# Performance work log

Measured on AMD Instinct MI355X. Metric: run time of the kernel, lower is better.

## Reference

```python
import jax, jax.numpy as jnp
import numpy as np

B, S, H, NH = 8, 1024, 1024, 16
D = H // NH          # attention_hidden_size = 64
V = S                # v_size must equal seq_len (mask broadcast)


def setup_inputs() -> dict:
    key = jax.random.key(0)
    ks = jax.random.split(key, 9)
    s = 0.02
    return {
        "q": jax.random.normal(ks[0], (B, S, H), jnp.float32),
        "k": jax.random.normal(ks[1], (B, S, H), jnp.float32),
        "v": jax.random.normal(ks[2], (B, S, H), jnp.float32),
        # per-head Q/K projections, stacked over heads: (NH, H, D)
        "Wq": jax.random.normal(ks[3], (NH, H, D), jnp.float32) * s,
        "bq": jax.random.normal(ks[4], (NH, D), jnp.float32) * s,
        "Wk": jax.random.normal(ks[5], (NH, H, D), jnp.float32) * s,
        "bk": jax.random.normal(ks[6], (NH, D), jnp.float32) * s,
        # shared V projection hidden -> v_size
        "Wv": jax.random.normal(ks[7], (H, V), jnp.float32) * s,
        "bv": jax.random.normal(ks[8], (V,), jnp.float32) * s,
    }


def reference(q, k, v, Wq, bq, Wk, bk, Wv, bv):
    d = Wq.shape[-1]
    scale = d ** (-0.5)
    # per-head projections, heads vectorized into leading axis n
    qh = jnp.einsum('bsh,nhd->nbsd', q, Wq) + bq[:, None, None, :]
    kh = jnp.einsum('bth,nhd->nbtd', k, Wk) + bk[:, None, None, :]
    vv = jnp.einsum('bth,hv->btv', v, Wv) + bv          # shared V: (B,S,V)
    seq = q.shape[1]
    mask = jnp.triu(jnp.full((seq, seq), -jnp.inf, dtype=q.dtype), 1)
    scores = jnp.einsum('nbsd,nbtd->nbst', qh, kh) * scale + mask
    p = jax.nn.softmax(scores, axis=-1)                  # (NH,B,S,S)
    # matmul against shared V then mean over heads (== stack + mean)
    out = jnp.einsum('nbst,btv->nbsv', p, vv).mean(axis=0)
    return out
```

## Files before the change

kernel.cpp:

```cpp
#include <hip/hip_runtime.h>


#define NHEAD 16
#define BATCH 8
#define SEQ   1024
#define HID   1024
#define DHEAD 64

typedef _Float16 f16;
typedef _Float16 f16x4 __attribute__((ext_vector_type(4)));
typedef _Float16 f16x8 __attribute__((ext_vector_type(8)));
typedef float    f32x4 __attribute__((ext_vector_type(4)));

__device__ __forceinline__ f32x4 mfma16(f16x8 a, f16x8 b, f32x4 c) {
  return __builtin_amdgcn_mfma_f32_16x16x32_f16(a, b, c, 0, 0, 0);
}

__device__ __forceinline__ void gload16(const f16* g, f16* l) {
  __builtin_amdgcn_global_load_lds(
      (const __attribute__((address_space(1))) void*)g,
      (__attribute__((address_space(3))) void*)l, 16, 0, 0);
}

__device__ __forceinline__ void stage_swz(const f16* __restrict__ g, int ldg,
                                          f16* lds, int nch, int tid,
                                          int step = 256) {
  for (int idx = tid; idx < nch; idx += step) {
    int row = idx >> 3, c16 = idx & 7;
    int sc = c16 ^ (row & 7);
    gload16(g + (size_t)row * ldg + sc * 8, lds + (size_t)(idx & ~63) * 8);
  }
}

__device__ __forceinline__ f16x8 lds_frag(const f16* lds, int row, int c16) {
  int sc = c16 ^ (row & 7);
  return *(const f16x8*)&lds[row * 64 + sc * 8];
}


__global__ __launch_bounds__(256) void conv3(
    const float* __restrict__ q, const float* __restrict__ k,
    const float* __restrict__ v, f16* __restrict__ dq, f16* __restrict__ dk,
    f16* __restrict__ dv) {
  const float* src = blockIdx.z == 0 ? q : blockIdx.z == 1 ? k : v;
  f16* dst = blockIdx.z == 0 ? dq : blockIdx.z == 1 ? dk : dv;
  int i = (blockIdx.x * 256 + threadIdx.x) * 4;
  float4 f = *(const float4*)(src + i);
  f16x4 o = { (f16)f.x, (f16)f.y, (f16)f.z, (f16)f.w };
  *(f16x4*)(dst + i) = o;
}

__global__ __launch_bounds__(256) void tconv2(
    const float* __restrict__ s0, const float* __restrict__ s1,
    f16* __restrict__ d0, f16* __restrict__ d1, int R, int C, int half) {
  int z = blockIdx.z;
  const float* src; f16* dst;
  if (z < half) { src = s0 + (size_t)z * R * C; dst = d0 + (size_t)z * R * C; }
  else { src = s1 + (size_t)(z - half) * R * C; dst = d1 + (size_t)(z - half) * R * C; }
  const int c0 = blockIdx.x * 64, r0 = blockIdx.y * 64;
  __shared__ f16 t[64][72];
  const int tid = threadIdx.x;
#pragma unroll
  for (int i = 0; i < 4; i++) {
    int chunk = tid + i * 256;
    int row = chunk >> 4, c4 = chunk & 15;
    float4 f = *(const float4*)&src[(size_t)(r0 + row) * C + c0 + c4 * 4];
    f16x4 h = { (f16)f.x, (f16)f.y, (f16)f.z, (f16)f.w };
    *(f16x4*)&t[row][c4 * 4] = h;
  }
  __syncthreads();
  const int cc = tid >> 2, q = tid & 3;
  f16 tmp[16];
#pragma unroll
  for (int j = 0; j < 16; j++) tmp[j] = t[q * 16 + j][cc];
  *(f16x8*)&dst[(size_t)(c0 + cc) * R + r0 + q * 16] = *(f16x8*)&tmp[0];
  *(f16x8*)&dst[(size_t)(c0 + cc) * R + r0 + q * 16 + 8] = *(f16x8*)&tmp[8];
}


__device__ __forceinline__ void gemm_core(
    const f16* __restrict__ A, const f16* __restrict__ Bt, int K, int Kend,
    int row0, int col0, f16* la, f16* lb, int tid, f32x4 (&acc)[4][4]) {
  const int lane = tid & 63;
  const int wr = (tid >> 6) >> 1, wc = (tid >> 6) & 1;
  for (int k0 = 0; k0 < Kend; k0 += 64) {
    __syncthreads();
    stage_swz(A + (size_t)row0 * K + k0, K, la, 1024, tid);
    stage_swz(Bt + (size_t)col0 * K + k0, K, lb, 1024, tid);
    __syncthreads();
#pragma unroll
    for (int ks = 0; ks < 2; ks++) {
      f16x8 af[4], bfr[4];
#pragma unroll
      for (int mi = 0; mi < 4; mi++)
        af[mi] = lds_frag(la, wr * 64 + mi * 16 + (lane & 15), ks * 4 + (lane >> 4));
#pragma unroll
      for (int ni = 0; ni < 4; ni++)
        bfr[ni] = lds_frag(lb, wc * 64 + ni * 16 + (lane & 15), ks * 4 + (lane >> 4));
#pragma unroll
      for (int mi = 0; mi < 4; mi++)
#pragma unroll
        for (int ni = 0; ni < 4; ni++)
          acc[mi][ni] = mfma16(af[mi], bfr[ni], acc[mi][ni]);
    }
  }
}


__global__ __launch_bounds__(256) void proj_gemm(
    const f16* __restrict__ A0, const f16* __restrict__ A1,
    const f16* __restrict__ Bt0, const f16* __restrict__ Bt1,
    const float* __restrict__ bias0, const float* __restrict__ bias1,
    f16* __restrict__ C0, f16* __restrict__ C1) {
  const int which = blockIdx.z;
  const f16* A = which ? A1 : A0;
  const f16* Bt = which ? Bt1 : Bt0;
  const float* bias = which ? bias1 : bias0;
  f16* C = which ? C1 : C0;
  __shared__ alignas(16) f16 la[128 * 64];
  __shared__ alignas(16) f16 lb[128 * 64];
  const int tid = threadIdx.x, lane = tid & 63;
  const int wr = (tid >> 6) >> 1, wc = (tid >> 6) & 1;
  const int row0 = blockIdx.x * 128, col0 = blockIdx.y * 128;
  f32x4 acc[4][4];
#pragma unroll
  for (int i = 0; i < 4; i++)
#pragma unroll
    for (int j = 0; j < 4; j++) acc[i][j] = (f32x4){0.f, 0.f, 0.f, 0.f};
  gemm_core(A, Bt, HID, HID, row0, col0, la, lb, tid, acc);
#pragma unroll
  for (int mi = 0; mi < 4; mi++)
#pragma unroll
    for (int ni = 0; ni < 4; ni++)
#pragma unroll
      for (int r = 0; r < 4; r++) {
        int m = row0 + wr * 64 + mi * 16 + ((lane >> 4) << 2) + r;
        int j = col0 + wc * 64 + ni * 16 + (lane & 15);
        float val = acc[mi][ni][r] + bias[j];
        int bb = m >> 10, s = m & 1023, hn = j >> 6, d = j & 63;
        C[(((size_t)hn * BATCH + bb) * SEQ + s) * DHEAD + d] = (f16)val;
      }
}


__global__ __launch_bounds__(256) void vv_gemm(
    const f16* __restrict__ A, const f16* __restrict__ Bt,
    const float* __restrict__ bias, f16* __restrict__ C) {
  __shared__ alignas(16) f16 la[128 * 64];
  __shared__ alignas(16) f16 lb[128 * 64];
  const int tid = threadIdx.x, lane = tid & 63;
  const int wr = (tid >> 6) >> 1, wc = (tid >> 6) & 1;
  const int row0 = blockIdx.x * 128, col0 = blockIdx.y * 128;
  f32x4 acc[4][4];
#pragma unroll
  for (int i = 0; i < 4; i++)
#pragma unroll
    for (int j = 0; j < 4; j++) acc[i][j] = (f32x4){0.f, 0.f, 0.f, 0.f};
  gemm_core(A, Bt, HID, HID, row0, col0, la, lb, tid, acc);
#pragma unroll
  for (int mi = 0; mi < 4; mi++)
#pragma unroll
    for (int ni = 0; ni < 4; ni++)
#pragma unroll
      for (int r = 0; r < 4; r++) {
        int m = row0 + wr * 64 + mi * 16 + ((lane >> 4) << 2) + r;
        int j = col0 + wc * 64 + ni * 16 + (lane & 15);
        float val = acc[mi][ni][r] + bias[m];
        int bb = j >> 10, t = j & 1023;
        C[((size_t)bb * SEQ + m) * SEQ + t] = (f16)val;
      }
}


__global__ __launch_bounds__(256) void attn_stats(
    const f16* __restrict__ QH, const f16* __restrict__ KH,
    float* __restrict__ madj_ws) {
  const int flat = blockIdx.x;
  const int sb = 15 - (flat >> 7);
  const int nb = flat & 127;
  const int n = nb >> 3, b = nb & 7;
  const int s0 = sb * 64;
  const f16* qh = QH + ((size_t)n * BATCH + b) * SEQ * DHEAD;
  const f16* kh = KH + ((size_t)n * BATCH + b) * SEQ * DHEAD;

  const int tid = threadIdx.x, lane = tid & 63, wave = tid >> 6;
  const int lr = lane & 15;
  const int qg = lane >> 4;
  const int ch = qg << 3;

  f16x8 aq[4][2];
#pragma unroll
  for (int fi = 0; fi < 4; fi++) {
    const f16* qp = qh + (size_t)(s0 + fi * 16 + lr) * 64 + ch;
    aq[fi][0] = *(const f16x8*)qp;
    aq[fi][1] = *(const f16x8*)(qp + 32);
  }

  const float sl2e = 0.125f * 1.44269504088896f;
  float l_p[16];
#pragma unroll
  for (int i = 0; i < 16; i++) l_p[i] = 0.f;

  const int nt = (sb + 1) * 4;
  const int dstart = sb * 4;
  const int njw = (nt - wave + 3) >> 2;
  const f16* kp = kh + (size_t)lr * 64 + ch;

  f16x8 kA0, kA1, kB0, kB1;

#define LDK(jj, X0, X1) { const f16* p_ = kp + (size_t)(jj) * 1024; \
    X0 = *(const f16x8*)p_; X1 = *(const f16x8*)(p_ + 32); }

#define COMP(jj, X0, X1) { \
    f32x4 c_[4]; \
    _Pragma("unroll") for (int fi = 0; fi < 4; fi++) { \
      f32x4 cc = (f32x4){0.f, 0.f, 0.f, 0.f}; \
      cc = mfma16(aq[fi][0], X0, cc); cc = mfma16(aq[fi][1], X1, cc); \
      c_[fi] = cc; } \
    if ((jj) < dstart) { \
      _Pragma("unroll") for (int fi = 0; fi < 4; fi++) \
        _Pragma("unroll") for (int r = 0; r < 4; r++) \
          l_p[fi * 4 + r] += exp2f(c_[fi][r] * sl2e); \
    } else { \
      int tg_ = (jj) * 16 + lr; \
      _Pragma("unroll") for (int fi = 0; fi < 4; fi++) \
        _Pragma("unroll") for (int r = 0; r < 4; r++) { \
          int sg_ = s0 + fi * 16 + qg * 4 + r; \
          l_p[fi * 4 + r] += (tg_ <= sg_) ? exp2f(c_[fi][r] * sl2e) : 0.f; } } }

  LDK(wave, kA0, kA1);
  int idx = 0;
  for (; idx + 2 <= njw; idx += 2) {
    LDK(wave + (idx + 1) * 4, kB0, kB1);
    COMP(wave + idx * 4, kA0, kA1);
    if (idx + 2 < njw) LDK(wave + (idx + 2) * 4, kA0, kA1);
    COMP(wave + (idx + 1) * 4, kB0, kB1);
  }
  if (idx < njw) COMP(wave + idx * 4, kA0, kA1);
#undef LDK
#undef COMP

  __shared__ float lds_l[4][64];
#pragma unroll
  for (int i = 0; i < 16; i++) {
    float l = l_p[i];
    l += __shfl_xor(l, 1); l += __shfl_xor(l, 2);
    l += __shfl_xor(l, 4); l += __shfl_xor(l, 8);
    if (lr == 0) lds_l[wave][(i >> 2) * 16 + qg * 4 + (i & 3)] = l;
  }
  __syncthreads();
  if (tid < 64) {
    float l = lds_l[0][tid] + lds_l[1][tid] + lds_l[2][tid] + lds_l[3][tid];
    madj_ws[((size_t)n * BATCH + b) * SEQ + s0 + tid] = -__log2f(l) - 4.0f;
  }
}


__global__ __launch_bounds__(512, 4) void pbar_gemm(
    const f16* __restrict__ QH, const f16* __restrict__ KH,
    const float* __restrict__ madj_ws, f16* __restrict__ pp) {
  const int flat = blockIdx.x;
  const int wg = (flat & 7) * 72 + (flat >> 3);
  const int y = wg / 36;
  int rb = 0, cb = 0;
  {
    int t = wg % 36;
#pragma unroll
    for (int r = 0; r < 8; ++r) {
      if (t <= r) { rb = r; cb = t; break; }
      t -= r + 1;
    }
  }
  const int r0 = rb * 128, c0 = cb * 128;
  const int b = y >> 1, g = y & 1;
  const int n0 = g * 8;
  const bool diag = (rb == cb);

  __shared__ alignas(16) f16 la[2][128 * 64];
  __shared__ alignas(16) f16 lb[2][128 * 64];

  const int tid = threadIdx.x, lane = tid & 63;
  const int wave = tid >> 6;
  const int wr = wave >> 2, wc = wave & 3;
  const int lr = lane & 15, qg = lane >> 4;
  const float sl2e = 0.125f * 1.44269504088896f;
  const size_t HS = (size_t)BATCH * SEQ * DHEAD;
  const f16* qbase = QH + ((size_t)n0 * BATCH + b) * SEQ * DHEAD + (size_t)r0 * 64;
  const f16* kbase = KH + ((size_t)n0 * BATCH + b) * SEQ * DHEAD + (size_t)c0 * 64;
  const float* mbase = madj_ws + ((size_t)n0 * BATCH + b) * SEQ + r0 +
                       wr * 64 + qg * 4;

  f32x4 pacc[4][2];
#pragma unroll
  for (int i = 0; i < 4; i++)
#pragma unroll
    for (int j = 0; j < 2; j++) pacc[i][j] = (f32x4){0.f, 0.f, 0.f, 0.f};

  stage_swz(qbase, 64, la[0], 1024, tid, 512);
  stage_swz(kbase, 64, lb[0], 1024, tid, 512);
  __syncthreads();

  for (int h = 0; h < 8; ++h) {
    const int cur = h & 1;
    if (h + 1 < 8) {
      stage_swz(qbase + (size_t)(h + 1) * HS, 64, la[cur ^ 1], 1024, tid, 512);
      stage_swz(kbase + (size_t)(h + 1) * HS, 64, lb[cur ^ 1], 1024, tid, 512);
    }
    const float* mb = mbase + (size_t)h * BATCH * SEQ;
    float4 m4[4];
#pragma unroll
    for (int mi = 0; mi < 4; mi++) m4[mi] = *(const float4*)(mb + mi * 16);

    f32x4 acc[4][2];
#pragma unroll
    for (int i = 0; i < 4; i++)
#pragma unroll
      for (int j = 0; j < 2; j++) acc[i][j] = (f32x4){0.f, 0.f, 0.f, 0.f};

#pragma unroll
    for (int ks = 0; ks < 2; ks++) {
      f16x8 af[4], bfr[2];
#pragma unroll
      for (int mi = 0; mi < 4; mi++)
        af[mi] = lds_frag(la[cur], wr * 64 + mi * 16 + lr, ks * 4 + qg);
#pragma unroll
      for (int ni = 0; ni < 2; ni++)
        bfr[ni] = lds_frag(lb[cur], wc * 32 + ni * 16 + lr, ks * 4 + qg);
#pragma unroll
      for (int mi = 0; mi < 4; mi++)
#pragma unroll
        for (int ni = 0; ni < 2; ni++)
          acc[mi][ni] = mfma16(af[mi], bfr[ni], acc[mi][ni]);
    }

#pragma unroll
    for (int mi = 0; mi < 4; mi++) {
      float ma[4] = {m4[mi].x, m4[mi].y, m4[mi].z, m4[mi].w};
#pragma unroll
      for (int ni = 0; ni < 2; ni++) {
        int tg = c0 + wc * 32 + ni * 16 + lr;
#pragma unroll
        for (int r = 0; r < 4; r++) {
          float p = exp2f(fmaf(acc[mi][ni][r], sl2e, ma[r]));
          if (diag) {
            int sg = r0 + wr * 64 + mi * 16 + qg * 4 + r;
            p = (tg <= sg) ? p : 0.f;
          }
          pacc[mi][ni][r] += p;
        }
      }
    }
    __syncthreads();
  }

  f16* out = pp + ((size_t)g * BATCH + b) * SEQ * SEQ;
#pragma unroll
  for (int mi = 0; mi < 4; mi++)
#pragma unroll
    for (int ni = 0; ni < 2; ni++)
#pragma unroll
      for (int r = 0; r < 4; r++) {
        int m = r0 + wr * 64 + mi * 16 + qg * 4 + r;
        int j = c0 + wc * 32 + ni * 16 + lr;
        out[(size_t)m * SEQ + j] = (f16)pacc[mi][ni][r];
      }
}


__global__ __launch_bounds__(256) void pv_gemm(
    const f16* __restrict__ pp, const f16* __restrict__ vvT,
    float* __restrict__ out) {
  const int b = blockIdx.z;
  const size_t GS = (size_t)BATCH * SEQ * SEQ;
  const f16* A0 = pp + (size_t)b * SEQ * SEQ;
  const f16* A1 = pp + GS + (size_t)b * SEQ * SEQ;
  const f16* Bt = vvT + (size_t)b * SEQ * SEQ;
  __shared__ alignas(16) f16 la0[128 * 64];
  __shared__ alignas(16) f16 la1[128 * 64];
  __shared__ alignas(16) f16 lb[128 * 64];
  const int tid = threadIdx.x, lane = tid & 63;
  const int wr = (tid >> 6) >> 1, wc = (tid >> 6) & 1;
  const int row0 = blockIdx.x * 128, col0 = blockIdx.y * 128;
  const int Kend = (row0 + 128 < SEQ) ? row0 + 128 : SEQ;

  f32x4 acc[4][4];
#pragma unroll
  for (int i = 0; i < 4; i++)
#pragma unroll
    for (int j = 0; j < 4; j++) acc[i][j] = (f32x4){0.f, 0.f, 0.f, 0.f};

  for (int k0 = 0; k0 < Kend; k0 += 64) {
    __syncthreads();
    stage_swz(A0 + (size_t)row0 * SEQ + k0, SEQ, la0, 1024, tid);
    stage_swz(A1 + (size_t)row0 * SEQ + k0, SEQ, la1, 1024, tid);
    stage_swz(Bt + (size_t)col0 * SEQ + k0, SEQ, lb, 1024, tid);
    __syncthreads();
#pragma unroll
    for (int ks = 0; ks < 2; ks++) {
      f16x8 a0[4], a1[4], bfr[4];
#pragma unroll
      for (int mi = 0; mi < 4; mi++) {
        a0[mi] = lds_frag(la0, wr * 64 + mi * 16 + (lane & 15), ks * 4 + (lane >> 4));
        a1[mi] = lds_frag(la1, wr * 64 + mi * 16 + (lane & 15), ks * 4 + (lane >> 4));
      }
#pragma unroll
      for (int ni = 0; ni < 4; ni++)
        bfr[ni] = lds_frag(lb, wc * 64 + ni * 16 + (lane & 15), ks * 4 + (lane >> 4));
#pragma unroll
      for (int mi = 0; mi < 4; mi++)
#pragma unroll
        for (int ni = 0; ni < 4; ni++) {
          acc[mi][ni] = mfma16(a0[mi], bfr[ni], acc[mi][ni]);
          acc[mi][ni] = mfma16(a1[mi], bfr[ni], acc[mi][ni]);
        }
    }
  }

#pragma unroll
  for (int mi = 0; mi < 4; mi++)
#pragma unroll
    for (int ni = 0; ni < 4; ni++)
#pragma unroll
      for (int r = 0; r < 4; r++) {
        int m = row0 + wr * 64 + mi * 16 + ((lane >> 4) << 2) + r;
        int j = col0 + wc * 64 + ni * 16 + (lane & 15);
        out[(size_t)b * SEQ * SEQ + (size_t)m * SEQ + j] = acc[mi][ni][r];
      }
}


extern "C" void kernel_launch(void* const* d_in, const int* in_sizes, int n_in,
                              void* d_out, int out_size, void* d_ws, size_t ws_size,
                              hipStream_t stream) {
  (void)in_sizes; (void)n_in; (void)out_size; (void)ws_size;
  const float* q  = (const float*)d_in[0];
  const float* k  = (const float*)d_in[1];
  const float* v  = (const float*)d_in[2];
  const float* Wq = (const float*)d_in[3];
  const float* bq = (const float*)d_in[4];
  const float* Wk = (const float*)d_in[5];
  const float* bk = (const float*)d_in[6];
  const float* Wv = (const float*)d_in[7];
  const float* bv = (const float*)d_in[8];
  float* out = (float*)d_out;

  const size_t EL  = (size_t)BATCH * SEQ * HID;
  const size_t WEL = (size_t)NHEAD * HID * DHEAD;

  char* ws = (char*)d_ws;
  f16* qbf = (f16*)ws;  ws += EL * 2;
  f16* kbf = (f16*)ws;  ws += EL * 2;
  f16* vbf = (f16*)ws;  ws += EL * 2;
  f16* WqT = (f16*)ws;  ws += WEL * 2;
  f16* WkT = (f16*)ws;  ws += WEL * 2;
  f16* WvT = (f16*)ws;  ws += WEL * 2;
  f16* QHb = (f16*)ws;  ws += EL * 2;
  f16* KHb = (f16*)ws;  ws += EL * 2;
  f16* vvT = (f16*)ws;  ws += EL * 2;
  float* madj_ws = (float*)ws; ws += (size_t)NHEAD * BATCH * SEQ * 4;
  f16* pp = qbf;

  conv3<<<dim3(8192, 1, 3), 256, 0, stream>>>(q, k, v, qbf, kbf, vbf);
  tconv2<<<dim3(1, 16, 32), 256, 0, stream>>>(Wq, Wk, WqT, WkT, 1024, 64, 16);
  tconv2<<<dim3(16, 16, 1), 256, 0, stream>>>(Wv, Wv, WvT, WvT, 1024, 1024, 1);

  proj_gemm<<<dim3(64, 8, 2), 256, 0, stream>>>(qbf, kbf, WqT, WkT, bq, bk,
                                                QHb, KHb);
  vv_gemm<<<dim3(8, 64, 1), 256, 0, stream>>>(WvT, vbf, bv, vvT);

  attn_stats<<<dim3(2048, 1, 1), 256, 0, stream>>>(QHb, KHb, madj_ws);
  pbar_gemm<<<dim3(576, 1, 1), 512, 0, stream>>>(QHb, KHb, madj_ws, pp);
  pv_gemm<<<dim3(8, 8, 8), 256, 0, stream>>>(pp, vvT, out);
}
```

Measured before the change: 225.8 us.

## Double-buffer LDS and use 8 waves in projection GEMMs

The projection and V GEMMs now use two LDS buffers so the next K-slice loads while MFMAs run on the current one, removing one barrier per step. Blocks grow to 512 threads with each wave owning a 64x32 sub-tile. This aims to hide global-load latency and raise occupancy, at the cost of doubled LDS per block (64KB) and fewer accumulators per wave.

```diff
diff --git a/kernel.cpp b/kernel.cpp
--- a/kernel.cpp
+++ b/kernel.cpp
@@ -78,36 +78,47 @@
 }
 
 
-__device__ __forceinline__ void gemm_core(
+__device__ __forceinline__ void gemm_core512(
     const f16* __restrict__ A, const f16* __restrict__ Bt, int K, int Kend,
-    int row0, int col0, f16* la, f16* lb, int tid, f32x4 (&acc)[4][4]) {
+    int row0, int col0, f16 (*la)[128 * 64], f16 (*lb)[128 * 64], int tid,
+    f32x4 (&acc)[4][2]) {
   const int lane = tid & 63;
-  const int wr = (tid >> 6) >> 1, wc = (tid >> 6) & 1;
-  for (int k0 = 0; k0 < Kend; k0 += 64) {
+  const int wave = tid >> 6;
+  const int wr = wave >> 2, wc = wave & 3;
+  const int lr = lane & 15, qg = lane >> 4;
+
+  stage_swz(A + (size_t)row0 * K, K, la[0], 1024, tid, 512);
+  stage_swz(Bt + (size_t)col0 * K, K, lb[0], 1024, tid, 512);
+  __syncthreads();
+
+  const int nsteps = Kend >> 6;
+  for (int st = 0; st < nsteps; ++st) {
+    const int cur = st & 1;
+    if (st + 1 < nsteps) {
+      stage_swz(A + (size_t)row0 * K + (st + 1) * 64, K, la[cur ^ 1], 1024, tid, 512);
+      stage_swz(Bt + (size_t)col0 * K + (st + 1) * 64, K, lb[cur ^ 1], 1024, tid, 512);
+    }
+#pragma unroll
+    for (int ks = 0; ks < 2; ks++) {
+      f16x8 af[4], bfr[2];
+#pragma unroll
+      for (int mi = 0; mi < 4; mi++)
+        af[mi] = lds_frag(la[cur], wr * 64 + mi * 16 + lr, ks * 4 + qg);
+#pragma unroll
+      for (int ni = 0; ni < 2; ni++)
+        bfr[ni] = lds_frag(lb[cur], wc * 32 + ni * 16 + lr, ks * 4 + qg);
+#pragma unroll
+      for (int mi = 0; mi < 4; mi++)
+#pragma unroll
+        for (int ni = 0; ni < 2; ni++)
+          acc[mi][ni] = mfma16(af[mi], bfr[ni], acc[mi][ni]);
+    }
     __syncthreads();
-    stage_swz(A + (size_t)row0 * K + k0, K, la, 1024, tid);
-    stage_swz(Bt + (size_t)col0 * K + k0, K, lb, 1024, tid);
-    __syncthreads();
-#pragma unroll
-    for (int ks = 0; ks < 2; ks++) {
-      f16x8 af[4], bfr[4];
-#pragma unroll
-      for (int mi = 0; mi < 4; mi++)
-        af[mi] = lds_frag(la, wr * 64 + mi * 16 + (lane & 15), ks * 4 + (lane >> 4));
-#pragma unroll
-      for (int ni = 0; ni < 4; ni++)
-        bfr[ni] = lds_frag(lb, wc * 64 + ni * 16 + (lane & 15), ks * 4 + (lane >> 4));
-#pragma unroll
-      for (int mi = 0; mi < 4; mi++)
-#pragma unroll
-        for (int ni = 0; ni < 4; ni++)
-          acc[mi][ni] = mfma16(af[mi], bfr[ni], acc[mi][ni]);
-    }
-  }
-}
-
-
-__global__ __launch_bounds__(256) void proj_gemm(
+  }
+}
+
+
+__global__ __launch_bounds__(512, 4) void proj_gemm(
     const f16* __restrict__ A0, const f16* __restrict__ A1,
     const f16* __restrict__ Bt0, const f16* __restrict__ Bt1,
     const float* __restrict__ bias0, const float* __restrict__ bias1,
@@ -117,25 +128,27 @@
   const f16* Bt = which ? Bt1 : Bt0;
   const float* bias = which ? bias1 : bias0;
   f16* C = which ? C1 : C0;
-  __shared__ alignas(16) f16 la[128 * 64];
-  __shared__ alignas(16) f16 lb[128 * 64];
+  __shared__ alignas(16) f16 la[2][128 * 64];
+  __shared__ alignas(16) f16 lb[2][128 * 64];
   const int tid = threadIdx.x, lane = tid & 63;
-  const int wr = (tid >> 6) >> 1, wc = (tid >> 6) & 1;
+  const int wave = tid >> 6;
+  const int wr = wave >> 2, wc = wave & 3;
+  const int lr = lane & 15, qg = lane >> 4;
   const int row0 = blockIdx.x * 128, col0 = blockIdx.y * 128;
-  f32x4 acc[4][4];
+  f32x4 acc[4][2];
 #pragma unroll
   for (int i = 0; i < 4; i++)
 #pragma unroll
-    for (int j = 0; j < 4; j++) acc[i][j] = (f32x4){0.f, 0.f, 0.f, 0.f};
-  gemm_core(A, Bt, HID, HID, row0, col0, la, lb, tid, acc);
+    for (int j = 0; j < 2; j++) acc[i][j] = (f32x4){0.f, 0.f, 0.f, 0.f};
+  gemm_core512(A, Bt, HID, HID, row0, col0, la, lb, tid, acc);
 #pragma unroll
   for (int mi = 0; mi < 4; mi++)
 #pragma unroll
-    for (int ni = 0; ni < 4; ni++)
+    for (int ni = 0; ni < 2; ni++)
 #pragma unroll
       for (int r = 0; r < 4; r++) {
-        int m = row0 + wr * 64 + mi * 16 + ((lane >> 4) << 2) + r;
-        int j = col0 + wc * 64 + ni * 16 + (lane & 15);
+        int m = row0 + wr * 64 + mi * 16 + qg * 4 + r;
+        int j = col0 + wc * 32 + ni * 16 + lr;
         float val = acc[mi][ni][r] + bias[j];
         int bb = m >> 10, s = m & 1023, hn = j >> 6, d = j & 63;
         C[(((size_t)hn * BATCH + bb) * SEQ + s) * DHEAD + d] = (f16)val;
@@ -143,28 +156,30 @@
 }
 
 
-__global__ __launch_bounds__(256) void vv_gemm(
+__global__ __launch_bounds__(512, 4) void vv_gemm(
     const f16* __restrict__ A, const f16* __restrict__ Bt,
     const float* __restrict__ bias, f16* __restrict__ C) {
-  __shared__ alignas(16) f16 la[128 * 64];
-  __shared__ alignas(16) f16 lb[128 * 64];
+  __shared__ alignas(16) f16 la[2][128 * 64];
+  __shared__ alignas(16) f16 lb[2][128 * 64];
   const int tid = threadIdx.x, lane = tid & 63;
-  const int wr = (tid >> 6) >> 1, wc = (tid >> 6) & 1;
+  const int wave = tid >> 6;
+  const int wr = wave >> 2, wc = wave & 3;
+  const int lr = lane & 15, qg = lane >> 4;
   const int row0 = blockIdx.x * 128, col0 = blockIdx.y * 128;
-  f32x4 acc[4][4];
+  f32x4 acc[4][2];
 #pragma unroll
   for (int i = 0; i < 4; i++)
 #pragma unroll
-    for (int j = 0; j < 4; j++) acc[i][j] = (f32x4){0.f, 0.f, 0.f, 0.f};
-  gemm_core(A, Bt, HID, HID, row0, col0, la, lb, tid, acc);
+    for (int j = 0; j < 2; j++) acc[i][j] = (f32x4){0.f, 0.f, 0.f, 0.f};
+  gemm_core512(A, Bt, HID, HID, row0, col0, la, lb, tid, acc);
 #pragma unroll
   for (int mi = 0; mi < 4; mi++)
 #pragma unroll
-    for (int ni = 0; ni < 4; ni++)
+    for (int ni = 0; ni < 2; ni++)
 #pragma unroll
       for (int r = 0; r < 4; r++) {
-        int m = row0 + wr * 64 + mi * 16 + ((lane >> 4) << 2) + r;
-        int j = col0 + wc * 64 + ni * 16 + (lane & 15);
+        int m = row0 + wr * 64 + mi * 16 + qg * 4 + r;
+        int j = col0 + wc * 32 + ni * 16 + lr;
         float val = acc[mi][ni][r] + bias[m];
         int bb = j >> 10, t = j & 1023;
         C[((size_t)bb * SEQ + m) * SEQ + t] = (f16)val;
@@ -464,9 +479,9 @@
   tconv2<<<dim3(1, 16, 32), 256, 0, stream>>>(Wq, Wk, WqT, WkT, 1024, 64, 16);
   tconv2<<<dim3(16, 16, 1), 256, 0, stream>>>(Wv, Wv, WvT, WvT, 1024, 1024, 1);
 
-  proj_gemm<<<dim3(64, 8, 2), 256, 0, stream>>>(qbf, kbf, WqT, WkT, bq, bk,
+  proj_gemm<<<dim3(64, 8, 2), 512, 0, stream>>>(qbf, kbf, WqT, WkT, bq, bk,
                                                 QHb, KHb);
-  vv_gemm<<<dim3(8, 64, 1), 256, 0, stream>>>(WvT, vbf, bv, vvT);
+  vv_gemm<<<dim3(8, 64, 1), 512, 0, stream>>>(WvT, vbf, bv, vvT);
 
   attn_stats<<<dim3(2048, 1, 1), 256, 0, stream>>>(QHb, KHb, madj_ws);
   pbar_gemm<<<dim3(576, 1, 1), 512, 0, stream>>>(QHb, KHb, madj_ws, pp);
```

Measured after the change: 231.9 us. 1.03x slower.

## Triple-buffer proj_gemm LDS loads with 512-thread blocks

Applied to the files above, without the earlier changes.

Rewrites the Q/K projection GEMM to use three LDS buffers with global-to-LDS prefetch two K-steps ahead. Each step waits on the vmcnt counter and issues a single barrier, where the shared gemm_core was used before. Block size doubles to 8 waves, each owning a 64x32 sub-tile, to hide load latency and raise parallelism within the block. Shared memory grows to 96 KB per block, which limits occupancy to about one block per CU. The hand-written vmcnt counts also depend on how many loads stage_swz issues per call.

```diff
diff --git a/kernel.cpp b/kernel.cpp
--- a/kernel.cpp
+++ b/kernel.cpp
@@ -107,7 +107,7 @@
 }
 
 
-__global__ __launch_bounds__(256) void proj_gemm(
+__global__ __launch_bounds__(512, 1) void proj_gemm(
     const f16* __restrict__ A0, const f16* __restrict__ A1,
     const f16* __restrict__ Bt0, const f16* __restrict__ Bt1,
     const float* __restrict__ bias0, const float* __restrict__ bias1,
@@ -117,25 +117,68 @@
   const f16* Bt = which ? Bt1 : Bt0;
   const float* bias = which ? bias1 : bias0;
   f16* C = which ? C1 : C0;
-  __shared__ alignas(16) f16 la[128 * 64];
-  __shared__ alignas(16) f16 lb[128 * 64];
+
+  __shared__ alignas(16) f16 la[3][128 * 64];
+  __shared__ alignas(16) f16 lb[3][128 * 64];
+
   const int tid = threadIdx.x, lane = tid & 63;
-  const int wr = (tid >> 6) >> 1, wc = (tid >> 6) & 1;
+  const int wave = tid >> 6;
+  const int wr = wave >> 2, wc = wave & 3;
+  const int lr = lane & 15, qg = lane >> 4;
   const int row0 = blockIdx.x * 128, col0 = blockIdx.y * 128;
-  f32x4 acc[4][4];
+  const f16* Arow = A + (size_t)row0 * HID;
+  const f16* Brow = Bt + (size_t)col0 * HID;
+
+  f32x4 acc[4][2];
 #pragma unroll
   for (int i = 0; i < 4; i++)
 #pragma unroll
-    for (int j = 0; j < 4; j++) acc[i][j] = (f32x4){0.f, 0.f, 0.f, 0.f};
-  gemm_core(A, Bt, HID, HID, row0, col0, la, lb, tid, acc);
+    for (int j = 0; j < 2; j++) acc[i][j] = (f32x4){0.f, 0.f, 0.f, 0.f};
+
+  stage_swz(Arow, HID, la[0], 1024, tid, 512);
+  stage_swz(Brow, HID, lb[0], 1024, tid, 512);
+  stage_swz(Arow + 64, HID, la[1], 1024, tid, 512);
+  stage_swz(Brow + 64, HID, lb[1], 1024, tid, 512);
+
+  int cur = 0, nxt2 = 2;
+  for (int t = 0; t < 16; ++t) {
+    if (t < 15) asm volatile("s_waitcnt vmcnt(4)" ::: "memory");
+    else        asm volatile("s_waitcnt vmcnt(0)" ::: "memory");
+    __builtin_amdgcn_s_barrier();
+    __builtin_amdgcn_sched_barrier(0);
+
+    if (t + 2 < 16) {
+      stage_swz(Arow + (t + 2) * 64, HID, la[nxt2], 1024, tid, 512);
+      stage_swz(Brow + (t + 2) * 64, HID, lb[nxt2], 1024, tid, 512);
+    }
+
+#pragma unroll
+    for (int ks = 0; ks < 2; ks++) {
+      f16x8 af[4], bfr[2];
+#pragma unroll
+      for (int mi = 0; mi < 4; mi++)
+        af[mi] = lds_frag(la[cur], wr * 64 + mi * 16 + lr, ks * 4 + qg);
+#pragma unroll
+      for (int ni = 0; ni < 2; ni++)
+        bfr[ni] = lds_frag(lb[cur], wc * 32 + ni * 16 + lr, ks * 4 + qg);
+#pragma unroll
+      for (int mi = 0; mi < 4; mi++)
+#pragma unroll
+        for (int ni = 0; ni < 2; ni++)
+          acc[mi][ni] = mfma16(af[mi], bfr[ni], acc[mi][ni]);
+    }
+    cur = cur == 2 ? 0 : cur + 1;
+    nxt2 = nxt2 == 2 ? 0 : nxt2 + 1;
+  }
+
 #pragma unroll
   for (int mi = 0; mi < 4; mi++)
 #pragma unroll
-    for (int ni = 0; ni < 4; ni++)
+    for (int ni = 0; ni < 2; ni++)
 #pragma unroll
       for (int r = 0; r < 4; r++) {
-        int m = row0 + wr * 64 + mi * 16 + ((lane >> 4) << 2) + r;
-        int j = col0 + wc * 64 + ni * 16 + (lane & 15);
+        int m = row0 + wr * 64 + mi * 16 + qg * 4 + r;
+        int j = col0 + wc * 32 + ni * 16 + lr;
         float val = acc[mi][ni][r] + bias[j];
         int bb = m >> 10, s = m & 1023, hn = j >> 6, d = j & 63;
         C[(((size_t)hn * BATCH + bb) * SEQ + s) * DHEAD + d] = (f16)val;
@@ -464,7 +507,7 @@
   tconv2<<<dim3(1, 16, 32), 256, 0, stream>>>(Wq, Wk, WqT, WkT, 1024, 64, 16);
   tconv2<<<dim3(16, 16, 1), 256, 0, stream>>>(Wv, Wv, WvT, WvT, 1024, 1024, 1);
 
-  proj_gemm<<<dim3(64, 8, 2), 256, 0, stream>>>(qbf, kbf, WqT, WkT, bq, bk,
+  proj_gemm<<<dim3(64, 8, 2), 512, 0, stream>>>(qbf, kbf, WqT, WkT, bq, bk,
                                                 QHb, KHb);
   vv_gemm<<<dim3(8, 64, 1), 256, 0, stream>>>(WvT, vbf, bv, vvT);
 
```

New measurement: 248.2 us. +9.9%, slower.
